# Optimization experiments

Hardware: AMD Instinct MI355X
Metric: run time of the kernel (lower is better)

Reference implementation:

```python
import jax, jax.numpy as jnp
import numpy as np

N_QUBITS = 12
LAYERS = 3


def _apply(state, mats, axes):
    """Apply batched k-qubit gate. state: [B]+[2]*n complex64; mats: [B, 2^k, 2^k]; axes: state axes (1-based)."""
    k = len(axes)
    d = 2 ** k
    s = jnp.moveaxis(state, axes, tuple(range(1, k + 1)))
    shp = s.shape
    s = jnp.einsum('bij,bjk->bik', mats, s.reshape(shp[0], d, -1))
    return jnp.moveaxis(s.reshape(shp), tuple(range(1, k + 1)), axes)


def _ry(theta):
    # RY(theta) = [[cos(t/2), -sin(t/2)], [sin(t/2), cos(t/2)]], batched over B
    c = jnp.cos(theta / 2).astype(jnp.complex64)
    s = jnp.sin(theta / 2).astype(jnp.complex64)
    return jnp.stack([jnp.stack([c, -s], -1), jnp.stack([s, c], -1)], -2)


def _crx(theta):
    # CRX: identity on control=0 subspace, RX(theta) on control=1 subspace (basis order |ct>)
    c = jnp.cos(theta / 2).astype(jnp.complex64)
    s = (-1j) * jnp.sin(theta / 2).astype(jnp.complex64)
    o = jnp.ones_like(c)
    z = jnp.zeros_like(c)
    rows = [[o, z, z, z], [z, o, z, z], [z, z, c, s], [z, z, s, c]]
    return jnp.stack([jnp.stack(r, -1) for r in rows], -2)


def _circuit(state_re, state_im, params):
    B = params.shape[0]
    n = N_QUBITS
    state = (state_re + 1j * state_im).astype(jnp.complex64).reshape((B,) + (2,) * n)
    p = params.reshape(B, LAYERS, 4, n)  # param idx order: RY block, CRX block, RY block, CRX block
    for l in range(LAYERS):
        th = p[:, l]
        for w in range(n):
            state = _apply(state, _ry(th[:, 0, w]), (w + 1,))
        for i, w in enumerate(reversed(range(n))):
            state = _apply(state, _crx(th[:, 1, i]), (w + 1, ((w + 1) % n) + 1))
        for w in range(n):
            state = _apply(state, _ry(th[:, 2, w]), (w + 1,))
        for i, w in enumerate([n - 1] + list(range(n - 1))):
            state = _apply(state, _crx(th[:, 3, i]), (w + 1, ((w - 1) % n) + 1))
    state = state.reshape(B, -1)
    return jnp.stack([state.real, state.imag], -1)  # [B, 2^n, 2]


def setup_inputs() -> dict:
    key = jax.random.key(0)
    k1, k2, k3 = jax.random.split(key, 3)
    B = 128
    dim = 2 ** N_QUBITS
    return {
        'state_re': jax.random.normal(k1, (B, dim), jnp.float32),
        'state_im': jax.random.normal(k2, (B, dim), jnp.float32),
        'params': jax.random.normal(k3, (B, LAYERS * 4 * N_QUBITS), jnp.float32),
    }


def reference(state_re, state_im, params):
    return _circuit(state_re, state_im, params)
```

## Files before the change

### kernel.cpp

```cpp
#include <hip/hip_runtime.h>
#include <math.h>

#define DIM  4096
#define BLK  256
#define NPAR 144

typedef float v2f __attribute__((ext_vector_type(2)));

struct Ph { int reg[4]; int wav[2]; };
struct TMap { unsigned pk[8]; unsigned short so[16]; unsigned short rn[16]; };

constexpr int REGS4[8][4] = {
  {11,0,1,2},{2,3,4,5},{5,6,7,8},{8,9,10,11},
  {10,11,0,1},{7,8,9,10},{4,5,6,7},{1,2,3,4}};
constexpr int PINS[8][2] = {
  {9,10},{9,10},{9,10},{2,3},{2,3},{2,3},{2,3},{9,10}};

constexpr Ph phaseAt(int i) {
  Ph p = {};
  int e = (i == 0) ? 0 : (i - 1) % 8;
  for (int j = 0; j < 4; ++j) p.reg[j] = REGS4[e][j];
  p.wav[0] = PINS[e][0]; p.wav[1] = PINS[e][1];
  return p;
}
constexpr bool inArr(const int* a, int n, int b) {
  for (int i = 0; i < n; ++i) if (a[i] == b) return true;
  return false;
}
constexpr int idxOf4(const int* a, int v) {
  for (int j = 0; j < 4; ++j) if (a[j] == v) return j;
  return -1;
}
constexpr bool isLoc(int t) {
  Ph a = phaseAt(t), b = phaseAt(t + 1);
  return a.wav[0]==b.wav[0] && a.wav[1]==b.wav[1];
}
constexpr int bufIdx(int t) {
  int k = 0;
  for (int u = 0; u <= t; ++u) if (!isLoc(u)) ++k;
  return (k + 1) & 1;
}
constexpr int sharedBit(Ph o, Ph n) {
  for (int j = 0; j < 4; ++j) if (inArr(n.reg, 4, o.reg[j])) return o.reg[j];
  return -1;
}

struct BuildOut { TMap m; int js, jn; bool ok; };

constexpr BuildOut buildT(Ph o, Ph n, bool local) {
  BuildOut R = {};
  R.ok = true;
  int s = sharedBit(o, n);
  if (s < 0) { R.ok = false; return R; }
  R.js = idxOf4(o.reg, s);
  R.jn = idxOf4(n.reg, s);
  if (R.js < 0 || R.jn < 0) { R.ok = false; return R; }
  bool lo[12] = {}, ln[12] = {};
  for (int b = 0; b < 12; ++b) {
    lo[b] = !inArr(o.reg,4,b) && !inArr(o.wav,2,b);
    ln[b] = !inArr(n.reg,4,b) && !inArr(n.wav,2,b);
  }
  int col[12] = {};
  bool uo[12] = {}, un[12] = {}, consumed[12] = {};
  col[s] = 1; consumed[s] = true;
  int row = 1;
  for (int b = 0; b < 12 && row < 4; ++b)
    if (lo[b] && ln[b] && !consumed[b]) { col[b] = 1 << row; uo[b]=un[b]=true; consumed[b]=true; ++row; }
  while (row < 4) {
    int a = -1, c = -1;
    for (int b = 0; b < 12; ++b) if (lo[b] && !uo[b] && !consumed[b]) { a = b; break; }
    for (int b = 0; b < 12; ++b) if (ln[b] && !un[b] && !consumed[b] && b != a) { c = b; break; }
    if (a < 0 || c < 0) { R.ok = false; return R; }
    col[a] |= 1 << row; col[c] |= 1 << row;
    uo[a]=true; un[c]=true; consumed[c]=true;
    ++row;
  }
  if (local) {
    for (int i = 0; i < 2; ++i) {
      if (consumed[o.wav[i]]) { R.ok = false; return R; }
      col[o.wav[i]] |= 1 << (10 + i);
      consumed[o.wav[i]] = true;
    }
    int rr = 4;
    for (int b = 0; b < 12; ++b) if (!consumed[b]) { col[b] |= 1 << rr; ++rr; }
    if (rr != 10) { R.ok = false; return R; }
  } else {
    int rr = 4;
    for (int b = 0; b < 12; ++b) if (!consumed[b]) { col[b] |= 1 << rr; ++rr; }
    if (rr != 12) { R.ok = false; return R; }
  }
  {
    int pv[12] = {}, pb[12] = {};
    int nr = 0;
    for (int b = 0; b < 12; ++b) {
      int v = col[b];
      for (int k = 0; k < nr; ++k) if (v & pb[k]) v ^= pv[k];
      if (v) { pb[nr] = v & (-v); pv[nr] = v; ++nr; }
    }
    if (nr != 12) { R.ok = false; return R; }
  }
  int Lo[6] = {}, Ln6[6] = {};
  int i0 = 0, i1 = 0;
  for (int b = 0; b < 12; ++b) { if (lo[b]) Lo[i0++] = b; if (ln[b]) Ln6[i1++] = b; }
  if (i0 != 6 || i1 != 6) { R.ok = false; return R; }
  for (int i = 0; i < 8; ++i) {
    unsigned po = (i < 6) ? (unsigned)col[Lo[i]] : (unsigned)col[o.wav[i-6]];
    unsigned pn = (i < 6) ? (unsigned)col[Ln6[i]] : (unsigned)col[n.wav[i-6]];
    R.m.pk[i] = po | (pn << 16);
  }
  for (int r = 0; r < 16; ++r) {
    int a = 0, c = 0;
    for (int j = 0; j < 4; ++j)
      if ((r >> j) & 1) { a ^= col[o.reg[j]]; c ^= col[n.reg[j]]; }
    R.m.so[r] = (unsigned short)(a * 8);
    R.m.rn[r] = (unsigned short)(c * 8);
  }
  return R;
}

constexpr bool mapsEqual(const TMap& a, const TMap& b) {
  for (int i = 0; i < 8; ++i) if (a.pk[i] != b.pk[i]) return false;
  for (int r = 0; r < 16; ++r)
    if (a.so[r] != b.so[r] || a.rn[r] != b.rn[r]) return false;
  return true;
}

struct AllT { TMap t[24]; bool loc[24]; int buf[24]; int js[24]; int jn[24]; bool ok; };
constexpr AllT buildAll() {
  AllT A = {};
  A.ok = true;
  for (int t = 0; t < 24; ++t) {
    BuildOut b = buildT(phaseAt(t), phaseAt(t + 1), isLoc(t));
    A.t[t] = b.m;
    A.ok = A.ok && b.ok;
    A.loc[t] = isLoc(t);
    A.buf[t] = bufIdx(t);
    A.js[t] = b.js;
    A.jn[t] = b.jn;
  }
  for (int t = 9; t < 24; ++t)
    A.ok = A.ok && mapsEqual(A.t[t], A.t[t-8]) && A.loc[t] == A.loc[t-8]
         && A.buf[t] == A.buf[t-8] && A.js[t] == A.js[t-8] && A.jn[t] == A.jn[t-8];
  {
    int ng = 0;
    for (int t = 1; t < 24; ++t) if (!A.loc[t]) ++ng;
    A.ok = A.ok && (ng == 6);
    for (int t = 1; t < 24; ++t) {
      bool expectGlob = (((t - 1) % 8) == 2) || (((t - 1) % 8) == 6);
      A.ok = A.ok && (A.loc[t] == !expectGlob);
    }
  }
  return A;
}
constexpr AllT AT = buildAll();
static_assert(AT.ok, "slot-map construction failed");

__device__ __forceinline__ float rlf(float v, int l) {
  return __int_as_float(__builtin_amdgcn_readlane(__float_as_int(v), l));
}
template<int AO>
__device__ __forceinline__ v2f angAt(const float (&ct)[3], const float (&st)[3]) {
  v2f a;
  a.x = rlf(ct[AO >> 6], AO & 63);
  a.y = rlf(st[AO >> 6], AO & 63);
  return a;
}

template<int J>
__device__ __forceinline__ void ry16(v2f (&z)[16], v2f a) {
  const float c = a.x, s = a.y;
  #pragma unroll
  for (int p = 0; p < 8; ++p) {
    const int r0 = ((p & ~((1 << J) - 1)) << 1) | (p & ((1 << J) - 1));
    const int r1 = r0 | (1 << J);
    v2f u = z[r0], v = z[r1];
    z[r0] = c * u - s * v;
    z[r1] = s * u + c * v;
  }
}
template<int JC, int JT>
__device__ __forceinline__ void crx16(v2f (&z)[16], v2f a) {
  const float c = a.x, s = a.y;
  constexpr int MC = 1 << JC, MT = 1 << JT;
  constexpr int mlo = MC < MT ? MC : MT;
  constexpr int mhi = MC < MT ? MT : MC;
  #pragma unroll
  for (int p = 0; p < 4; ++p) {
    int q = ((p & ~(mlo - 1)) << 1) | (p & (mlo - 1));
    q = ((q & ~(mhi - 1)) << 1) | (q & (mhi - 1));
    const int r0 = q | MC, r1 = r0 | MT;
    v2f u = z[r0], v = z[r1];
    v2f n0, n1;
    n0.x = c * u.x + s * v.y;
    n0.y = c * u.y - s * v.x;
    n1.x = c * v.x + s * u.y;
    n1.y = c * v.y - s * u.x;
    z[r0] = n0; z[r1] = n1;
  }
}

template<int E, int L>
__device__ __forceinline__ void gates(v2f (&z)[16], const float (&ct)[3], const float (&st)[3]) {
#define A(k) (angAt<48 * L + (k)>(ct, st))
  if constexpr (E == 0)      { ry16<0>(z,A(0));  ry16<1>(z,A(11)); ry16<2>(z,A(10)); ry16<3>(z,A(9));
                               crx16<1,0>(z,A(12)); crx16<2,1>(z,A(13)); crx16<3,2>(z,A(14)); }
  else if constexpr (E == 1) { ry16<1>(z,A(8));  ry16<2>(z,A(7));  ry16<3>(z,A(6));
                               crx16<1,0>(z,A(15)); crx16<2,1>(z,A(16)); crx16<3,2>(z,A(17)); }
  else if constexpr (E == 2) { ry16<1>(z,A(5));  ry16<2>(z,A(4));  ry16<3>(z,A(3));
                               crx16<1,0>(z,A(18)); crx16<2,1>(z,A(19)); crx16<3,2>(z,A(20)); }
  else if constexpr (E == 3) { ry16<1>(z,A(2));  ry16<2>(z,A(1));
                               crx16<1,0>(z,A(21)); crx16<2,1>(z,A(22)); crx16<3,2>(z,A(23)); }
  else if constexpr (E == 4) { ry16<0>(z,A(25)); ry16<1>(z,A(24)); ry16<2>(z,A(35)); ry16<3>(z,A(34));
                               crx16<2,3>(z,A(36)); crx16<1,2>(z,A(37)); crx16<0,1>(z,A(38)); }
  else if constexpr (E == 5) { ry16<0>(z,A(28)); ry16<1>(z,A(27)); ry16<2>(z,A(26));
                               crx16<2,3>(z,A(39)); crx16<1,2>(z,A(40)); crx16<0,1>(z,A(41)); }
  else if constexpr (E == 6) { ry16<0>(z,A(31)); ry16<1>(z,A(30)); ry16<2>(z,A(29));
                               crx16<2,3>(z,A(42)); crx16<1,2>(z,A(43)); crx16<0,1>(z,A(44)); }
  else                       { ry16<1>(z,A(33)); ry16<2>(z,A(32));
                               crx16<2,3>(z,A(45)); crx16<1,2>(z,A(46)); crx16<0,1>(z,A(47)); }
#undef A
}

template<int T>
__device__ __forceinline__ void restage(v2f (&z)[16],
                                        const unsigned (&bo)[8], const unsigned (&bn)[8],
                                        char* Lb, char* C0, char* C1) {
  constexpr int K = (T - 1) & 7;
  constexpr bool LOC = AT.loc[T];
  constexpr int JS = AT.js[T], JN = AT.jn[T];
  char* buf = LOC ? Lb : (AT.buf[T] ? C1 : C0);
  const unsigned o = bo[K], n_ = bn[K];
  #pragma unroll
  for (int r = 0; r < 16; ++r) {
    if (r & (1 << JS)) continue;
    v2f z0 = z[r], z1 = z[r | (1 << JS)];
    float4 w; w.x = z0.x; w.y = z0.y; w.z = z1.x; w.w = z1.y;
    *(float4*)(buf + (o ^ AT.t[T].so[r])) = w;
  }
  if (LOC) {
    asm volatile("" ::: "memory");
  } else {
    __syncthreads();
  }
  #pragma unroll
  for (int r = 0; r < 16; ++r) {
    if (r & (1 << JN)) continue;
    float4 w = *(const float4*)(buf + (n_ ^ AT.t[T].rn[r]));
    v2f z0, z1;
    z0.x = w.x; z0.y = w.y;
    z1.x = w.z; z1.y = w.w;
    z[r] = z0;
    z[r | (1 << JN)] = z1;
  }
}

template<int L>
__device__ __forceinline__ void layer(v2f (&z)[16],
                                      const unsigned (&bo)[8], const unsigned (&bn)[8],
                                      const float (&ct)[3], const float (&st)[3],
                                      char* Lb, char* C0, char* C1) {
  gates<0, L>(z, ct, st);  restage<8*L + 1>(z, bo, bn, Lb, C0, C1);
  gates<1, L>(z, ct, st);  restage<8*L + 2>(z, bo, bn, Lb, C0, C1);
  gates<2, L>(z, ct, st);  restage<8*L + 3>(z, bo, bn, Lb, C0, C1);
  gates<3, L>(z, ct, st);  restage<8*L + 4>(z, bo, bn, Lb, C0, C1);
  gates<4, L>(z, ct, st);  restage<8*L + 5>(z, bo, bn, Lb, C0, C1);
  gates<5, L>(z, ct, st);  restage<8*L + 6>(z, bo, bn, Lb, C0, C1);
  gates<6, L>(z, ct, st);  restage<8*L + 7>(z, bo, bn, Lb, C0, C1);
  gates<7, L>(z, ct, st);
  if constexpr (L < 2) restage<8*L + 8>(z, bo, bn, Lb, C0, C1);
}

__global__ __launch_bounds__(BLK) void ansatz_kernel(
    const float* __restrict__ sre, const float* __restrict__ sim,
    const float* __restrict__ params, float* __restrict__ out) {

  __shared__ alignas(16) v2f C0s[DIM], C1s[DIM], Ls[DIM];

  const int b = blockIdx.x, tid = threadIdx.x;
  char* C0 = (char*)C0s;
  char* C1 = (char*)C1s;
  char* Lb = (char*)Ls;

  float ct[3], st[3];
  {
    const int lane = tid & 63;
    #pragma unroll
    for (int j = 0; j < 3; ++j) {
      int idx = lane + 64 * j;
      int ci = (idx < NPAR) ? idx : 0;
      float th = params[(size_t)b * NPAR + ci];
      sincosf(0.5f * th, &st[j], &ct[j]);
    }
  }

  unsigned bo[8], bn[8];
  #pragma unroll
  for (int k = 0; k < 8; ++k) {
    unsigned acc = 0;
    #pragma unroll
    for (int i = 0; i < 8; ++i)
      acc ^= (unsigned)(-((tid >> i) & 1)) & AT.t[k + 1].pk[i];
    bo[k] = (acc & 0xfffu) << 3;
    bn[k] = ((acc >> 16) & 0xfffu) << 3;
  }

  v2f z[16];
  {
    const float4* pr = (const float4*)(sre + (size_t)b * DIM + (size_t)tid * 8);
    const float4* pi = (const float4*)(sim + (size_t)b * DIM + (size_t)tid * 8);
    float4 f0 = pr[0], f1 = pr[1], f2 = pr[512], f3 = pr[513];
    float4 g0 = pi[0], g1 = pi[1], g2 = pi[512], g3 = pi[513];
    z[0].x  = f0.x; z[0].y  = g0.x;  z[2].x  = f0.y; z[2].y  = g0.y;
    z[4].x  = f0.z; z[4].y  = g0.z;  z[6].x  = f0.w; z[6].y  = g0.w;
    z[8].x  = f1.x; z[8].y  = g1.x;  z[10].x = f1.y; z[10].y = g1.y;
    z[12].x = f1.z; z[12].y = g1.z;  z[14].x = f1.w; z[14].y = g1.w;
    z[1].x  = f2.x; z[1].y  = g2.x;  z[3].x  = f2.y; z[3].y  = g2.y;
    z[5].x  = f2.z; z[5].y  = g2.z;  z[7].x  = f2.w; z[7].y  = g2.w;
    z[9].x  = f3.x; z[9].y  = g3.x;  z[11].x = f3.y; z[11].y = g3.y;
    z[13].x = f3.z; z[13].y = g3.z;  z[15].x = f3.w; z[15].y = g3.w;
  }

  layer<0>(z, bo, bn, ct, st, Lb, C0, C1);
  layer<1>(z, bo, bn, ct, st, Lb, C0, C1);
  layer<2>(z, bo, bn, ct, st, Lb, C0, C1);

  {
    int base = (tid & 1) | ((tid & 2) << 4) | ((tid & 4) << 4)
             | ((tid & 8) << 4) | ((tid & 16) << 4) | ((tid & 32) << 6)
             | ((tid & 64) << 3) | ((tid & 128) << 3);
    v2f* o2 = (v2f*)out + (size_t)b * DIM + base;
    #pragma unroll
    for (int r = 0; r < 16; ++r)
      o2[2 * r] = z[r];
  }
}

extern "C" void kernel_launch(void* const* d_in, const int* in_sizes, int n_in,
                              void* d_out, int out_size, void* d_ws, size_t ws_size,
                              hipStream_t stream) {
  const float* sre    = (const float*)d_in[0];
  const float* sim    = (const float*)d_in[1];
  const float* params = (const float*)d_in[2];
  float* out          = (float*)d_out;

  const int B = in_sizes[0] / DIM;
  ansatz_kernel<<<B, BLK, 0, stream>>>(sre, sim, params, out);
}
```

Baseline: 81.70 us.

## Pack two batch items per block and single-buffer the cross-wave exchange

Each 512-thread block now processes two circuit instances, one per 256-thread half, so only 64 blocks are launched. The double-buffered cross-wave shared buffer is replaced by a single buffer with a second barrier after the read-back. The CRX update is also rewritten as packed v2f arithmetic. This halves the block count (fewer CUs used for B=128) and adds an extra __syncthreads per global restage, while block-wide barriers now couple two independent items.

```diff
diff --git a/kernel.cpp b/kernel.cpp
--- a/kernel.cpp
+++ b/kernel.cpp
@@ -2,7 +2,7 @@
 #include <math.h>
 
 #define DIM  4096
-#define BLK  256
+#define BLK  512
 #define NPAR 144
 
 typedef float v2f __attribute__((ext_vector_type(2)));
@@ -34,11 +34,6 @@
 constexpr bool isLoc(int t) {
   Ph a = phaseAt(t), b = phaseAt(t + 1);
   return a.wav[0]==b.wav[0] && a.wav[1]==b.wav[1];
-}
-constexpr int bufIdx(int t) {
-  int k = 0;
-  for (int u = 0; u <= t; ++u) if (!isLoc(u)) ++k;
-  return (k + 1) & 1;
 }
 constexpr int sharedBit(Ph o, Ph n) {
   for (int j = 0; j < 4; ++j) if (inArr(n.reg, 4, o.reg[j])) return o.reg[j];
@@ -125,7 +120,7 @@
   return true;
 }
 
-struct AllT { TMap t[24]; bool loc[24]; int buf[24]; int js[24]; int jn[24]; bool ok; };
+struct AllT { TMap t[24]; bool loc[24]; int js[24]; int jn[24]; bool ok; };
 constexpr AllT buildAll() {
   AllT A = {};
   A.ok = true;
@@ -134,13 +129,12 @@
     A.t[t] = b.m;
     A.ok = A.ok && b.ok;
     A.loc[t] = isLoc(t);
-    A.buf[t] = bufIdx(t);
     A.js[t] = b.js;
     A.jn[t] = b.jn;
   }
   for (int t = 9; t < 24; ++t)
     A.ok = A.ok && mapsEqual(A.t[t], A.t[t-8]) && A.loc[t] == A.loc[t-8]
-         && A.buf[t] == A.buf[t-8] && A.js[t] == A.js[t-8] && A.jn[t] == A.jn[t-8];
+         && A.js[t] == A.js[t-8] && A.jn[t] == A.jn[t-8];
   {
     int ng = 0;
     for (int t = 1; t < 24; ++t) if (!A.loc[t]) ++ng;
@@ -181,6 +175,7 @@
 template<int JC, int JT>
 __device__ __forceinline__ void crx16(v2f (&z)[16], v2f a) {
   const float c = a.x, s = a.y;
+  const v2f spm = {s, -s};
   constexpr int MC = 1 << JC, MT = 1 << JT;
   constexpr int mlo = MC < MT ? MC : MT;
   constexpr int mhi = MC < MT ? MT : MC;
@@ -190,12 +185,10 @@
     q = ((q & ~(mhi - 1)) << 1) | (q & (mhi - 1));
     const int r0 = q | MC, r1 = r0 | MT;
     v2f u = z[r0], v = z[r1];
-    v2f n0, n1;
-    n0.x = c * u.x + s * v.y;
-    n0.y = c * u.y - s * v.x;
-    n1.x = c * v.x + s * u.y;
-    n1.y = c * v.y - s * u.x;
-    z[r0] = n0; z[r1] = n1;
+    v2f vs = {v.y, v.x};
+    v2f us = {u.y, u.x};
+    z[r0] = c * u + spm * vs;
+    z[r1] = c * v + spm * us;
   }
 }
 
@@ -224,11 +217,11 @@
 template<int T>
 __device__ __forceinline__ void restage(v2f (&z)[16],
                                         const unsigned (&bo)[8], const unsigned (&bn)[8],
-                                        char* Lb, char* C0, char* C1) {
+                                        char* Lb, char* Cb) {
   constexpr int K = (T - 1) & 7;
   constexpr bool LOC = AT.loc[T];
   constexpr int JS = AT.js[T], JN = AT.jn[T];
-  char* buf = LOC ? Lb : (AT.buf[T] ? C1 : C0);
+  char* buf = LOC ? Lb : Cb;
   const unsigned o = bo[K], n_ = bn[K];
   #pragma unroll
   for (int r = 0; r < 16; ++r) {
@@ -252,38 +245,42 @@
     z[r] = z0;
     z[r | (1 << JN)] = z1;
   }
+  if constexpr (!LOC) {
+    __syncthreads();
+  }
 }
 
 template<int L>
 __device__ __forceinline__ void layer(v2f (&z)[16],
                                       const unsigned (&bo)[8], const unsigned (&bn)[8],
                                       const float (&ct)[3], const float (&st)[3],
-                                      char* Lb, char* C0, char* C1) {
-  gates<0, L>(z, ct, st);  restage<8*L + 1>(z, bo, bn, Lb, C0, C1);
-  gates<1, L>(z, ct, st);  restage<8*L + 2>(z, bo, bn, Lb, C0, C1);
-  gates<2, L>(z, ct, st);  restage<8*L + 3>(z, bo, bn, Lb, C0, C1);
-  gates<3, L>(z, ct, st);  restage<8*L + 4>(z, bo, bn, Lb, C0, C1);
-  gates<4, L>(z, ct, st);  restage<8*L + 5>(z, bo, bn, Lb, C0, C1);
-  gates<5, L>(z, ct, st);  restage<8*L + 6>(z, bo, bn, Lb, C0, C1);
-  gates<6, L>(z, ct, st);  restage<8*L + 7>(z, bo, bn, Lb, C0, C1);
+                                      char* Lb, char* Cb) {
+  gates<0, L>(z, ct, st);  restage<8*L + 1>(z, bo, bn, Lb, Cb);
+  gates<1, L>(z, ct, st);  restage<8*L + 2>(z, bo, bn, Lb, Cb);
+  gates<2, L>(z, ct, st);  restage<8*L + 3>(z, bo, bn, Lb, Cb);
+  gates<3, L>(z, ct, st);  restage<8*L + 4>(z, bo, bn, Lb, Cb);
+  gates<4, L>(z, ct, st);  restage<8*L + 5>(z, bo, bn, Lb, Cb);
+  gates<5, L>(z, ct, st);  restage<8*L + 6>(z, bo, bn, Lb, Cb);
+  gates<6, L>(z, ct, st);  restage<8*L + 7>(z, bo, bn, Lb, Cb);
   gates<7, L>(z, ct, st);
-  if constexpr (L < 2) restage<8*L + 8>(z, bo, bn, Lb, C0, C1);
+  if constexpr (L < 2) restage<8*L + 8>(z, bo, bn, Lb, Cb);
 }
 
 __global__ __launch_bounds__(BLK) void ansatz_kernel(
     const float* __restrict__ sre, const float* __restrict__ sim,
     const float* __restrict__ params, float* __restrict__ out) {
 
-  __shared__ alignas(16) v2f C0s[DIM], C1s[DIM], Ls[DIM];
-
-  const int b = blockIdx.x, tid = threadIdx.x;
-  char* C0 = (char*)C0s;
-  char* C1 = (char*)C1s;
-  char* Lb = (char*)Ls;
+  __shared__ alignas(16) v2f Cs[2][DIM], Lss[2][DIM];
+
+  const int st8 = threadIdx.x >> 8;
+  const int tid = threadIdx.x & 255;
+  const int b = blockIdx.x * 2 + st8;
+  char* Cb = (char*)&Cs[st8][0];
+  char* Lb = (char*)&Lss[st8][0];
 
   float ct[3], st[3];
   {
-    const int lane = tid & 63;
+    const int lane = threadIdx.x & 63;
     #pragma unroll
     for (int j = 0; j < 3; ++j) {
       int idx = lane + 64 * j;
@@ -320,9 +317,9 @@
     z[13].x = f3.z; z[13].y = g3.z;  z[15].x = f3.w; z[15].y = g3.w;
   }
 
-  layer<0>(z, bo, bn, ct, st, Lb, C0, C1);
-  layer<1>(z, bo, bn, ct, st, Lb, C0, C1);
-  layer<2>(z, bo, bn, ct, st, Lb, C0, C1);
+  layer<0>(z, bo, bn, ct, st, Lb, Cb);
+  layer<1>(z, bo, bn, ct, st, Lb, Cb);
+  layer<2>(z, bo, bn, ct, st, Lb, Cb);
 
   {
     int base = (tid & 1) | ((tid & 2) << 4) | ((tid & 4) << 4)
@@ -344,5 +341,5 @@
   float* out          = (float*)d_out;
 
   const int B = in_sizes[0] / DIM;
-  ansatz_kernel<<<B, BLK, 0, stream>>>(sre, sim, params, out);
-}
+  ansatz_kernel<<<B / 2, BLK, 0, stream>>>(sre, sim, params, out);
+}
```

Result: slower. 90.02 us (+10.2%).
